# Kernel tuning notes

Measured on AMD Instinct MI355X. Metric: run time of the kernel, lower is better.

The kernel has to match this reference:

```python
import jax, jax.numpy as jnp
import numpy as np

BETA = 1.0  # init kwarg beta
TAU = 0.5   # init kwarg tau


def setup_inputs() -> dict:
    key = jax.random.key(0)
    k1, k2, k3, k4, k5 = jax.random.split(key, 5)
    M, N, D = 6, 2048, 1152  # views, batch, flattened feature dim (Linear(1152,128))
    return {
        "x_all": jax.random.normal(k1, (M, N, D), jnp.float32),
        "W": jax.random.normal(k2, (D, 128), jnp.float32) * 0.03,  # line_layers weight (in,out)
        "b": jax.random.normal(k3, (128,), jnp.float32) * 0.01,    # line_layers bias
        "U": jax.random.normal(k4, (128, 64), jnp.float32),
        "V": jax.random.normal(k5, (128, 64), jnp.float32),
    }


def _retrieve(x, P):
    # x: [M, N, 128], P: [128, 64]
    # per-sample: P @ softmax(beta * (P.T @ x_i))  ==  softmax(beta * x @ P) @ P.T  (batched)
    attn = jax.nn.softmax(BETA * jnp.einsum('mnd,dk->mnk', x, P), axis=-1)  # [M,N,64]
    return jnp.einsum('mnk,dk->mnd', attn, P)  # [M,N,128]


def _pair_loss_sum(E):
    # E: [M, N, 128]. Sum of losses over all ordered pairs of distinct views.
    M, N = E.shape[0], E.shape[1]
    sim = jnp.einsum('mnd,kpd->mknp', E, E) / TAU          # [M,M,N,N]
    pos = jnp.diagonal(sim, axis1=2, axis2=3)              # [M,M,N] positives (diag)
    # negatives = off-diagonal entries of each row; exclude diag via -inf for stable logsumexp
    neg = jnp.where(jnp.eye(N, dtype=bool), -jnp.inf, sim)
    lse = jax.nn.logsumexp(neg, axis=-1)                   # [M,M,N]
    # -log(exp(pos)/sum(exp(neg))) == lse - pos
    per_pair = (lse - pos).mean(axis=-1)                   # [M,M]
    off_diag = 1.0 - jnp.eye(M, dtype=per_pair.dtype)      # skip i == j (torch.equal check)
    return (per_pair * off_diag).sum()


def reference(x_all, W, b, U, V):
    M, N = x_all.shape[0], x_all.shape[1]
    x = x_all.reshape(M, N, -1) @ W + b                    # Linear(1152, 128)
    Ue = _retrieve(x, U)
    Ve = _retrieve(x, V)
    total = _pair_loss_sum(Ue) + _pair_loss_sum(Ve)
    return total / (2 * M * (M - 1))
```

## Files before the change

### kernel.cpp

```cpp
#include <hip/hip_runtime.h>
#include <hip/hip_bf16.h>

#define M_VIEWS 6
#define N_ROWS  2048
#define D_IN    1152
#define D_HID   128
#define D_K     64
#define TOT_ROWS (M_VIEWS * N_ROWS)
#define SCALE_E 1.6986436f
#define LOG2E   1.4426950408889634f

typedef short bf16x8 __attribute__((ext_vector_type(8)));
typedef float f32x4  __attribute__((ext_vector_type(4)));

typedef __attribute__((address_space(1))) const void gvoid_t;
typedef __attribute__((address_space(3))) void svoid_t;

__device__ inline void async16(const void* g, void* l) {
    __builtin_amdgcn_global_load_lds((gvoid_t*)g, (svoid_t*)l, 16, 0, 0);
}

#if __has_builtin(__builtin_amdgcn_exp2f)
__device__ inline float fexp2(float x) { return __builtin_amdgcn_exp2f(x); }
#else
__device__ inline float fexp2(float x) { return exp2f(x); }
#endif
#if __has_builtin(__builtin_amdgcn_logf)
__device__ inline float flog2(float x) { return __builtin_amdgcn_logf(x); }
#else
__device__ inline float flog2(float x) { return log2f(x); }
#endif

__device__ inline short2 splitf(float v) {
    __hip_bfloat16 hb = __float2bfloat16(v);
    float rem = v - __bfloat162float(hb);
    __hip_bfloat16 lb = __float2bfloat16(rem);
    short2 r;
    r.x = *reinterpret_cast<const short*>(&hb);
    r.y = *reinterpret_cast<const short*>(&lb);
    return r;
}

__device__ inline short bf16of(float v) {
    __hip_bfloat16 hb = __float2bfloat16(v);
    return *reinterpret_cast<const short*>(&hb);
}

__global__ __launch_bounds__(64) void prep_kernel(
    const float* __restrict__ W,
    const float* __restrict__ U, const float* __restrict__ V,
    __hip_bfloat16* __restrict__ Whi,
    __hip_bfloat16* __restrict__ Pfhi, __hip_bfloat16* __restrict__ Pflo)
{
    const int lane = threadIdx.x;
    const int lg = lane >> 4, lr = lane & 15;

    if (blockIdx.x < 288) {
        const int s  = blockIdx.x >> 3;
        const int ct = blockIdx.x & 7;
        bf16x8 hi;
        #pragma unroll
        for (int i = 0; i < 8; ++i)
            hi[i] = bf16of(W[(size_t)(s * 32 + lg * 8 + i) * D_HID + ct * 16 + lr]);
        size_t off = ((size_t)(s * 8 + ct) * 64 + lane) * 8;
        *reinterpret_cast<bf16x8*>(Whi + off) = hi;
    } else {
        const int blk = blockIdx.x - 288;
        const int mat = blk >> 5, f = blk & 31;
        const float* P = mat ? V : U;
        bf16x8 hi, lo;
        #pragma unroll
        for (int i = 0; i < 8; ++i) {
            float w;
            if (f < 16) {
                int s = f >> 2, ct = f & 3;
                w = P[(size_t)(s * 32 + lg * 8 + i) * D_K + ct * 16 + lr] * LOG2E;
            } else {
                int g = f - 16, s2 = g >> 3, ct2 = g & 7;
                w = P[(size_t)(ct2 * 16 + lr) * D_K + s2 * 32 + lg * 8 + i];
            }
            short2 hl = splitf(w);
            hi[i] = hl.x; lo[i] = hl.y;
        }
        size_t off = ((size_t)(mat * 32 + f) * 64 + lane) * 8;
        *reinterpret_cast<bf16x8*>(Pfhi + off) = hi;
        *reinterpret_cast<bf16x8*>(Pflo + off) = lo;
    }
}

__global__ __launch_bounds__(512) void xretrieve_kernel(
    const float* __restrict__ xall,
    const __hip_bfloat16* __restrict__ Whi,
    const float* __restrict__ bias,
    const __hip_bfloat16* __restrict__ Pfhi,
    const __hip_bfloat16* __restrict__ Pflo,
    __hip_bfloat16* __restrict__ E)
{
    __shared__ __align__(16) char smem[32768 + 8448 + 9216];
    f32x4* red = reinterpret_cast<f32x4*>(smem);
    float* xs  = reinterpret_cast<float*>(smem + 32768);
    float* alb = reinterpret_cast<float*>(smem + 32768 + 8448);

    const int wave = threadIdx.x >> 6, lane = threadIdx.x & 63;
    const int lg = lane >> 4, lr = lane & 15;
    const int row0 = blockIdx.x * 16;

    const int nst = (wave < 4) ? 5 : 4;
    const int st0 = (wave < 4) ? wave * 5 : 20 + (wave - 4) * 4;
    const float* ap = xall + (size_t)(row0 + lr) * D_IN + st0 * 32;

    f32x4 acc[8];
    #pragma unroll
    for (int ct = 0; ct < 8; ++ct) acc[ct] = {0.f, 0.f, 0.f, 0.f};

    const bf16x8* whb = reinterpret_cast<const bf16x8*>(Whi) + lane;
    for (int s = 0; s < nst; ++s) {
        const int gs = st0 + s;
        const float* a8 = ap + s * 32 + lg * 8;
        float4 va = *reinterpret_cast<const float4*>(a8);
        float4 vb = *reinterpret_cast<const float4*>(a8 + 4);
        bf16x8 ah;
        ah[0] = bf16of(va.x); ah[1] = bf16of(va.y);
        ah[2] = bf16of(va.z); ah[3] = bf16of(va.w);
        ah[4] = bf16of(vb.x); ah[5] = bf16of(vb.y);
        ah[6] = bf16of(vb.z); ah[7] = bf16of(vb.w);
        #pragma unroll
        for (int ct = 0; ct < 8; ++ct) {
            bf16x8 wh = whb[(size_t)(gs * 8 + ct) * 64];
            acc[ct] = __builtin_amdgcn_mfma_f32_16x16x32_bf16(ah, wh, acc[ct], 0, 0, 0);
        }
    }

    if (wave >= 4) {
        #pragma unroll
        for (int ct = 0; ct < 8; ++ct)
            red[(wave - 4) * 512 + ct * 64 + lane] = acc[ct];
    }
    __syncthreads();
    if (wave < 4) {
        #pragma unroll
        for (int ct = 0; ct < 8; ++ct)
            acc[ct] += red[wave * 512 + ct * 64 + lane];
    }
    __syncthreads();
    if (wave >= 1 && wave < 4) {
        #pragma unroll
        for (int ct = 0; ct < 8; ++ct)
            red[(wave - 1) * 512 + ct * 64 + lane] = acc[ct];
    }
    __syncthreads();
    if (wave == 0) {
        #pragma unroll
        for (int ct = 0; ct < 8; ++ct) {
            f32x4 a = acc[ct];
            a += red[ct * 64 + lane];
            a += red[512 + ct * 64 + lane];
            a += red[1024 + ct * 64 + lane];
            float bj = bias[ct * 16 + lr];
            #pragma unroll
            for (int j = 0; j < 4; ++j)
                xs[(lg * 4 + j) * 132 + ct * 16 + lr] = a[j] + bj;
        }
    }
    __syncthreads();

    if (wave < 2) {
        const int mat = wave;
        bf16x8 xh[4], xl[4];
        #pragma unroll
        for (int s = 0; s < 4; ++s) {
            const float* xp = xs + lr * 132 + s * 32 + lg * 8;
            float4 va = *reinterpret_cast<const float4*>(xp);
            float4 vb = *reinterpret_cast<const float4*>(xp + 4);
            float v[8] = {va.x, va.y, va.z, va.w, vb.x, vb.y, vb.z, vb.w};
            #pragma unroll
            for (int i = 0; i < 8; ++i) {
                short2 hl = splitf(v[i]);
                xh[s][i] = hl.x; xl[s][i] = hl.y;
            }
        }

        const bf16x8* bh = reinterpret_cast<const bf16x8*>(Pfhi) + (size_t)mat * 32 * 64 + lane;
        const bf16x8* bl = reinterpret_cast<const bf16x8*>(Pflo) + (size_t)mat * 32 * 64 + lane;

        f32x4 lacc[4];
        #pragma unroll
        for (int ct = 0; ct < 4; ++ct) lacc[ct] = {0.f, 0.f, 0.f, 0.f};
        #pragma unroll
        for (int ct = 0; ct < 4; ++ct) {
            #pragma unroll
            for (int s = 0; s < 4; ++s) {
                bf16x8 wh = bh[(s * 4 + ct) * 64];
                bf16x8 wl = bl[(s * 4 + ct) * 64];
                lacc[ct] = __builtin_amdgcn_mfma_f32_16x16x32_bf16(xh[s], wh, lacc[ct], 0, 0, 0);
                lacc[ct] = __builtin_amdgcn_mfma_f32_16x16x32_bf16(xl[s], wh, lacc[ct], 0, 0, 0);
                lacc[ct] = __builtin_amdgcn_mfma_f32_16x16x32_bf16(xh[s], wl, lacc[ct], 0, 0, 0);
            }
        }

        float* al = alb + mat * (16 * 72);
        #pragma unroll
        for (int j = 0; j < 4; ++j) {
            float l0 = lacc[0][j], l1 = lacc[1][j], l2 = lacc[2][j], l3 = lacc[3][j];
            float mx = fmaxf(fmaxf(l0, l1), fmaxf(l2, l3));
            #pragma unroll
            for (int s = 1; s < 16; s <<= 1) mx = fmaxf(mx, __shfl_xor(mx, s));
            float p0 = fexp2(l0 - mx), p1 = fexp2(l1 - mx);
            float p2 = fexp2(l2 - mx), p3 = fexp2(l3 - mx);
            float sm = p0 + p1 + p2 + p3;
            #pragma unroll
            for (int s = 1; s < 16; s <<= 1) sm += __shfl_xor(sm, s);
            float inv = 1.0f / sm;
            float* ar = al + (lg * 4 + j) * 72;
            ar[lr]      = p0 * inv;
            ar[16 + lr] = p1 * inv;
            ar[32 + lr] = p2 * inv;
            ar[48 + lr] = p3 * inv;
        }
    }
    __syncthreads();

    {
        const int mat2 = wave & 1;
        const int cp   = wave >> 1;
        const float* al = alb + mat2 * (16 * 72);
        const bf16x8* bh = reinterpret_cast<const bf16x8*>(Pfhi) + (size_t)mat2 * 32 * 64 + lane;
        const bf16x8* bl = reinterpret_cast<const bf16x8*>(Pflo) + (size_t)mat2 * 32 * 64 + lane;

        bf16x8 aah[2], aal[2];
        #pragma unroll
        for (int s2 = 0; s2 < 2; ++s2) {
            const float* ap2 = al + lr * 72 + s2 * 32 + lg * 8;
            float4 va = *reinterpret_cast<const float4*>(ap2);
            float4 vb = *reinterpret_cast<const float4*>(ap2 + 4);
            float v[8] = {va.x, va.y, va.z, va.w, vb.x, vb.y, vb.z, vb.w};
            #pragma unroll
            for (int i = 0; i < 8; ++i) {
                short2 hl = splitf(v[i]);
                aah[s2][i] = hl.x; aal[s2][i] = hl.y;
            }
        }

        __hip_bfloat16* Er = E + ((size_t)mat2 * TOT_ROWS + row0) * D_HID;
        #pragma unroll
        for (int q = 0; q < 2; ++q) {
            const int ct2 = cp * 2 + q;
            f32x4 eacc = {0.f, 0.f, 0.f, 0.f};
            #pragma unroll
            for (int s2 = 0; s2 < 2; ++s2) {
                bf16x8 wh = bh[(16 + s2 * 8 + ct2) * 64];
                bf16x8 wl = bl[(16 + s2 * 8 + ct2) * 64];
                eacc = __builtin_amdgcn_mfma_f32_16x16x32_bf16(aah[s2], wh, eacc, 0, 0, 0);
                eacc = __builtin_amdgcn_mfma_f32_16x16x32_bf16(aal[s2], wh, eacc, 0, 0, 0);
                eacc = __builtin_amdgcn_mfma_f32_16x16x32_bf16(aah[s2], wl, eacc, 0, 0, 0);
            }
            #pragma unroll
            for (int j = 0; j < 4; ++j)
                Er[(size_t)(lg * 4 + j) * D_HID + ct2 * 16 + lr] =
                    __float2bfloat16(eacc[j] * SCALE_E);
        }
    }
}

__global__ __launch_bounds__(512) void pair_lse_kernel(
    const __hip_bfloat16* __restrict__ E,
    float* __restrict__ partial)
{
    __shared__ __align__(16) unsigned char kbuf[2 * 16384];

    const int bid    = blockIdx.x;
    const int linear = (bid & 7) * 120 + (bid >> 3);
    const int half = linear & 1;
    const int qt   = (linear >> 1) & 7;
    const int job  = linear >> 4;
    const int mat = job / 30;
    const int pr  = job % 30;
    const int m   = pr / 5;
    int k = pr % 5; k += (k >= m);

    const __hip_bfloat16* Qm = E + ((size_t)(mat * M_VIEWS + m)) * N_ROWS * D_HID;
    const __hip_bfloat16* Kk = E + ((size_t)(mat * M_VIEWS + k)) * N_ROWS * D_HID;

    const int tid  = threadIdx.x;
    const int wave = tid >> 6, lane = tid & 63;
    const int lr = lane & 15, lg = lane >> 4;

    const int qrow0 = qt * 256 + wave * 32;

    bf16x8 afrag[2][4];
    #pragma unroll
    for (int rf = 0; rf < 2; ++rf) {
        const __hip_bfloat16* qp = Qm + (size_t)(qrow0 + rf * 16 + lr) * D_HID;
        #pragma unroll
        for (int s = 0; s < 4; ++s)
            afrag[rf][s] = *reinterpret_cast<const bf16x8*>(qp + s * 32 + lg * 8);
    }

    float mrun[2][4], lrun[2][4], pos[2][4];
    #pragma unroll
    for (int rf = 0; rf < 2; ++rf)
        #pragma unroll
        for (int j = 0; j < 4; ++j) {
            mrun[rf][j] = -1e30f; lrun[rf][j] = 0.f; pos[rf][j] = 0.f;
        }

    const int ptdiag = qt * 4 + (wave >> 1);
    const int ctd0   = (wave & 1) * 2;
    const int pt0    = half * 16;

    #define STAGE(pt, b)                                                        \
        {                                                                       \
            const char* base = (const char*)Kk + (size_t)(pt) * 16384;          \
            _Pragma("unroll")                                                   \
            for (int i = 0; i < 2; ++i) {                                       \
                int f = wave * 2 + i;                                           \
                int ct_ = f >> 2, s_ = f & 3;                                   \
                async16(base + (ct_ * 16 + lr) * 256 + s_ * 64 + lg * 16,       \
                        kbuf + (b) * 16384 + f * 1024);                         \
            }                                                                   \
        }

    STAGE(pt0, 0);
    __syncthreads();

    const unsigned char* kb0 = kbuf + lane * 16;
    for (int t = 0; t < 16; ++t) {
        const int pt = pt0 + t;
        if (t < 15) STAGE(pt + 1, (t + 1) & 1);

        const unsigned char* kb = kb0 + (t & 1) * 16384;
        f32x4 acc[2][4];
        #pragma unroll
        for (int rf = 0; rf < 2; ++rf)
            #pragma unroll
            for (int ct = 0; ct < 4; ++ct) acc[rf][ct] = {0.f, 0.f, 0.f, 0.f};

        #pragma unroll
        for (int ct = 0; ct < 4; ++ct) {
            #pragma unroll
            for (int s = 0; s < 4; ++s) {
                bf16x8 bf = *reinterpret_cast<const bf16x8*>(kb + (ct * 4 + s) * 1024);
                acc[0][ct] = __builtin_amdgcn_mfma_f32_16x16x32_bf16(afrag[0][s], bf, acc[0][ct], 0, 0, 0);
                acc[1][ct] = __builtin_amdgcn_mfma_f32_16x16x32_bf16(afrag[1][s], bf, acc[1][ct], 0, 0, 0);
            }
        }

        const bool dtile = (pt == ptdiag);
        #pragma unroll
        for (int rf = 0; rf < 2; ++rf) {
            #pragma unroll
            for (int j = 0; j < 4; ++j) {
                float v0 = acc[rf][0][j], v1 = acc[rf][1][j];
                float v2 = acc[rf][2][j], v3 = acc[rf][3][j];
                if (dtile) {
                    const int cd = ctd0 + rf;
                    const bool dl = (lr == lg * 4 + j);
                    float vd = (cd == 0) ? v0 : (cd == 1) ? v1 : (cd == 2) ? v2 : v3;
                    if (dl) {
                        pos[rf][j] = vd;
                        float nv = -INFINITY;
                        if      (cd == 0) v0 = nv;
                        else if (cd == 1) v1 = nv;
                        else if (cd == 2) v2 = nv;
                        else              v3 = nv;
                    }
                }
                float tmax = fmaxf(fmaxf(v0, v1), fmaxf(v2, v3));
                float nm = fmaxf(mrun[rf][j], tmax);
                float ps = fexp2(v0 - nm) + fexp2(v1 - nm)
                         + fexp2(v2 - nm) + fexp2(v3 - nm);
                lrun[rf][j] = lrun[rf][j] * fexp2(mrun[rf][j] - nm) + ps;
                mrun[rf][j] = nm;
            }
        }
        __syncthreads();
    }

    #pragma unroll
    for (int rf = 0; rf < 2; ++rf) {
        #pragma unroll
        for (int j = 0; j < 4; ++j) {
            float Mv = mrun[rf][j], Lv = lrun[rf][j];
            #pragma unroll
            for (int s = 1; s < 16; s <<= 1) {
                float Mo = __shfl_xor(Mv, s);
                float Lo = __shfl_xor(Lv, s);
                float nm = fmaxf(Mv, Mo);
                Lv = Lv * fexp2(Mv - nm) + Lo * fexp2(Mo - nm);
                Mv = nm;
            }
            float P = pos[rf][j];
            #pragma unroll
            for (int s = 1; s < 16; s <<= 1) P += __shfl_xor(P, s);
            if (lr == 0) {
                const int row = qrow0 + rf * 16 + lg * 4 + j;
                float* dst = partial + (((size_t)job * N_ROWS + row) * 2 + half) * 3;
                dst[0] = Mv; dst[1] = Lv; dst[2] = P;
            }
        }
    }
}

__global__ __launch_bounds__(256) void merge_kernel(
    const float* __restrict__ partial, float* __restrict__ out, float scale)
{
    __shared__ float wsum[4];
    const int r = blockIdx.x * 256 + threadIdx.x;
    const float* p = partial + (size_t)r * 6;
    float m0 = p[0], l0 = p[1], p0 = p[2];
    float m1 = p[3], l1 = p[4], p1 = p[5];
    float ms = fmaxf(m0, m1);
    float L  = l0 * fexp2(m0 - ms) + l1 * fexp2(m1 - ms);
    float c  = (ms + flog2(L)) - (p0 + p1);

    #pragma unroll
    for (int s = 1; s < 64; s <<= 1) c += __shfl_xor(c, s);
    const int wave = threadIdx.x >> 6, lane = threadIdx.x & 63;
    if (lane == 0) wsum[wave] = c;
    __syncthreads();
    if (threadIdx.x == 0)
        atomicAdd(out, (wsum[0] + wsum[1] + wsum[2] + wsum[3]) * scale);
}

extern "C" void kernel_launch(void* const* d_in, const int* in_sizes, int n_in,
                              void* d_out, int out_size, void* d_ws, size_t ws_size,
                              hipStream_t stream) {
    const float* xall = (const float*)d_in[0];
    const float* W    = (const float*)d_in[1];
    const float* b    = (const float*)d_in[2];
    const float* U    = (const float*)d_in[3];
    const float* V    = (const float*)d_in[4];
    float* out = (float*)d_out;

    char* ws = (char*)d_ws;
    __hip_bfloat16* E   = (__hip_bfloat16*)ws;
    __hip_bfloat16* Whi = E + 2 * (size_t)TOT_ROWS * D_HID;
    __hip_bfloat16* Pfhi = Whi + 36 * 8 * 64 * 8;
    __hip_bfloat16* Pflo = Pfhi + 2 * 32 * 64 * 8;
    float* partial = (float*)(Pflo + 2 * 32 * 64 * 8);

    (void)hipMemsetAsync(d_out, 0, sizeof(float), stream);

    prep_kernel<<<352, 64, 0, stream>>>(W, U, V, Whi, Pfhi, Pflo);
    xretrieve_kernel<<<TOT_ROWS / 16, 512, 0, stream>>>(xall, Whi, b, Pfhi, Pflo, E);

    pair_lse_kernel<<<960, 512, 0, stream>>>(E, partial);

    const float scale = 0.6931471805599453f / (2048.0f * 60.0f);
    merge_kernel<<<60 * 2048 / 256, 256, 0, stream>>>(partial, out, scale);
}
```

Baseline: 134.4 us.

## Drop key-split and merge kernel; shrink xretrieve block to four waves

pair_lse_kernel now sweeps all 32 key tiles per block instead of splitting keys into two halves. It finalizes the per-row logsumexp minus positive in-kernel and atomically adds a block sum to the output, which removes the partial buffer and the separate merge kernel launch. xretrieve_kernel drops from 8 waves to 4, each doing 9 K-steps, with a single reduction stage and the retrieval stage doing 4 column tiles per wave. The trade-off is half as many pair_lse blocks (480) with twice the serial work each, and fewer waves per xretrieve block to hide memory latency.

```diff
diff --git a/kernel.cpp b/kernel.cpp
--- a/kernel.cpp
+++ b/kernel.cpp
@@ -88,7 +88,7 @@
     }
 }
 
-__global__ __launch_bounds__(512) void xretrieve_kernel(
+__global__ __launch_bounds__(256) void xretrieve_kernel(
     const float* __restrict__ xall,
     const __hip_bfloat16* __restrict__ Whi,
     const float* __restrict__ bias,
@@ -96,26 +96,23 @@
     const __hip_bfloat16* __restrict__ Pflo,
     __hip_bfloat16* __restrict__ E)
 {
-    __shared__ __align__(16) char smem[32768 + 8448 + 9216];
+    __shared__ __align__(16) char smem[24576];
     f32x4* red = reinterpret_cast<f32x4*>(smem);
-    float* xs  = reinterpret_cast<float*>(smem + 32768);
-    float* alb = reinterpret_cast<float*>(smem + 32768 + 8448);
+    float* xs  = reinterpret_cast<float*>(smem);
+    float* alb = reinterpret_cast<float*>(smem + 8448);
 
     const int wave = threadIdx.x >> 6, lane = threadIdx.x & 63;
     const int lg = lane >> 4, lr = lane & 15;
     const int row0 = blockIdx.x * 16;
 
-    const int nst = (wave < 4) ? 5 : 4;
-    const int st0 = (wave < 4) ? wave * 5 : 20 + (wave - 4) * 4;
-    const float* ap = xall + (size_t)(row0 + lr) * D_IN + st0 * 32;
-
+    const float* ap = xall + (size_t)(row0 + lr) * D_IN + wave * 288;
     f32x4 acc[8];
     #pragma unroll
     for (int ct = 0; ct < 8; ++ct) acc[ct] = {0.f, 0.f, 0.f, 0.f};
 
     const bf16x8* whb = reinterpret_cast<const bf16x8*>(Whi) + lane;
-    for (int s = 0; s < nst; ++s) {
-        const int gs = st0 + s;
+    for (int s = 0; s < 9; ++s) {
+        const int gs = wave * 9 + s;
         const float* a8 = ap + s * 32 + lg * 8;
         float4 va = *reinterpret_cast<const float4*>(a8);
         float4 vb = *reinterpret_cast<const float4*>(a8 + 4);
@@ -131,25 +128,14 @@
         }
     }
 
-    if (wave >= 4) {
-        #pragma unroll
-        for (int ct = 0; ct < 8; ++ct)
-            red[(wave - 4) * 512 + ct * 64 + lane] = acc[ct];
-    }
-    __syncthreads();
-    if (wave < 4) {
-        #pragma unroll
-        for (int ct = 0; ct < 8; ++ct)
-            acc[ct] += red[wave * 512 + ct * 64 + lane];
-    }
-    __syncthreads();
-    if (wave >= 1 && wave < 4) {
+    if (wave > 0) {
         #pragma unroll
         for (int ct = 0; ct < 8; ++ct)
             red[(wave - 1) * 512 + ct * 64 + lane] = acc[ct];
     }
     __syncthreads();
     if (wave == 0) {
+        f32x4 xv[8];
         #pragma unroll
         for (int ct = 0; ct < 8; ++ct) {
             f32x4 a = acc[ct];
@@ -158,9 +144,16 @@
             a += red[1024 + ct * 64 + lane];
             float bj = bias[ct * 16 + lr];
             #pragma unroll
+            for (int j = 0; j < 4; ++j) xv[ct][j] = a[j] + bj;
+        }
+        __syncthreads();
+        #pragma unroll
+        for (int ct = 0; ct < 8; ++ct)
+            #pragma unroll
             for (int j = 0; j < 4; ++j)
-                xs[(lg * 4 + j) * 132 + ct * 16 + lr] = a[j] + bj;
-        }
+                xs[(lg * 4 + j) * 132 + ct * 16 + lr] = xv[ct][j];
+    } else {
+        __syncthreads();
     }
     __syncthreads();
 
@@ -243,8 +236,8 @@
 
         __hip_bfloat16* Er = E + ((size_t)mat2 * TOT_ROWS + row0) * D_HID;
         #pragma unroll
-        for (int q = 0; q < 2; ++q) {
-            const int ct2 = cp * 2 + q;
+        for (int q = 0; q < 4; ++q) {
+            const int ct2 = cp * 4 + q;
             f32x4 eacc = {0.f, 0.f, 0.f, 0.f};
             #pragma unroll
             for (int s2 = 0; s2 < 2; ++s2) {
@@ -264,15 +257,15 @@
 
 __global__ __launch_bounds__(512) void pair_lse_kernel(
     const __hip_bfloat16* __restrict__ E,
-    float* __restrict__ partial)
+    float* __restrict__ out, float scale)
 {
     __shared__ __align__(16) unsigned char kbuf[2 * 16384];
+    __shared__ float bsum[8];
 
     const int bid    = blockIdx.x;
-    const int linear = (bid & 7) * 120 + (bid >> 3);
-    const int half = linear & 1;
-    const int qt   = (linear >> 1) & 7;
-    const int job  = linear >> 4;
+    const int linear = (bid & 7) * 60 + (bid >> 3);
+    const int qt  = linear & 7;
+    const int job = linear >> 3;
     const int mat = job / 30;
     const int pr  = job % 30;
     const int m   = pr / 5;
@@ -306,7 +299,6 @@
 
     const int ptdiag = qt * 4 + (wave >> 1);
     const int ctd0   = (wave & 1) * 2;
-    const int pt0    = half * 16;
 
     #define STAGE(pt, b)                                                        \
         {                                                                       \
@@ -320,15 +312,15 @@
             }                                                                   \
         }
 
-    STAGE(pt0, 0);
+    STAGE(0, 0);
     __syncthreads();
 
     const unsigned char* kb0 = kbuf + lane * 16;
-    for (int t = 0; t < 16; ++t) {
-        const int pt = pt0 + t;
-        if (t < 15) STAGE(pt + 1, (t + 1) & 1);
-
-        const unsigned char* kb = kb0 + (t & 1) * 16384;
+    int buf = 0;
+    for (int pt = 0; pt < 32; ++pt) {
+        if (pt < 31) STAGE(pt + 1, buf ^ 1);
+
+        const unsigned char* kb = kb0 + buf * 16384;
         f32x4 acc[2][4];
         #pragma unroll
         for (int rf = 0; rf < 2; ++rf)
@@ -374,8 +366,10 @@
             }
         }
         __syncthreads();
-    }
-
+        buf ^= 1;
+    }
+
+    float contrib = 0.f;
     #pragma unroll
     for (int rf = 0; rf < 2; ++rf) {
         #pragma unroll
@@ -392,34 +386,20 @@
             float P = pos[rf][j];
             #pragma unroll
             for (int s = 1; s < 16; s <<= 1) P += __shfl_xor(P, s);
-            if (lr == 0) {
-                const int row = qrow0 + rf * 16 + lg * 4 + j;
-                float* dst = partial + (((size_t)job * N_ROWS + row) * 2 + half) * 3;
-                dst[0] = Mv; dst[1] = Lv; dst[2] = P;
-            }
-        }
-    }
-}
-
-__global__ __launch_bounds__(256) void merge_kernel(
-    const float* __restrict__ partial, float* __restrict__ out, float scale)
-{
-    __shared__ float wsum[4];
-    const int r = blockIdx.x * 256 + threadIdx.x;
-    const float* p = partial + (size_t)r * 6;
-    float m0 = p[0], l0 = p[1], p0 = p[2];
-    float m1 = p[3], l1 = p[4], p1 = p[5];
-    float ms = fmaxf(m0, m1);
-    float L  = l0 * fexp2(m0 - ms) + l1 * fexp2(m1 - ms);
-    float c  = (ms + flog2(L)) - (p0 + p1);
-
+            if (lr == 0) contrib += (Mv + flog2(Lv)) - P;
+        }
+    }
     #pragma unroll
-    for (int s = 1; s < 64; s <<= 1) c += __shfl_xor(c, s);
-    const int wave = threadIdx.x >> 6, lane = threadIdx.x & 63;
-    if (lane == 0) wsum[wave] = c;
+    for (int s = 1; s < 64; s <<= 1) contrib += __shfl_xor(contrib, s);
+
+    if (lane == 0) bsum[wave] = contrib;
     __syncthreads();
-    if (threadIdx.x == 0)
-        atomicAdd(out, (wsum[0] + wsum[1] + wsum[2] + wsum[3]) * scale);
+    if (tid == 0) {
+        float t = 0.f;
+        #pragma unroll
+        for (int w = 0; w < 8; ++w) t += bsum[w];
+        atomicAdd(out, t * scale);
+    }
 }
 
 extern "C" void kernel_launch(void* const* d_in, const int* in_sizes, int n_in,
@@ -437,15 +417,12 @@
     __hip_bfloat16* Whi = E + 2 * (size_t)TOT_ROWS * D_HID;
     __hip_bfloat16* Pfhi = Whi + 36 * 8 * 64 * 8;
     __hip_bfloat16* Pflo = Pfhi + 2 * 32 * 64 * 8;
-    float* partial = (float*)(Pflo + 2 * 32 * 64 * 8);
 
     (void)hipMemsetAsync(d_out, 0, sizeof(float), stream);
 
     prep_kernel<<<352, 64, 0, stream>>>(W, U, V, Whi, Pfhi, Pflo);
-    xretrieve_kernel<<<TOT_ROWS / 16, 512, 0, stream>>>(xall, Whi, b, Pfhi, Pflo, E);
-
-    pair_lse_kernel<<<960, 512, 0, stream>>>(E, partial);
+    xretrieve_kernel<<<TOT_ROWS / 16, 256, 0, stream>>>(xall, Whi, b, Pfhi, Pflo, E);
 
     const float scale = 0.6931471805599453f / (2048.0f * 60.0f);
-    merge_kernel<<<60 * 2048 / 256, 256, 0, stream>>>(partial, out, scale);
-}
+    pair_lse_kernel<<<480, 512, 0, stream>>>(E, out, scale);
+}
```

Result: faster. 124.2 us, median of 2 (-7.6%).
